# Kernel optimization log

Measured on AMD Instinct MI355X. Metric: run time of the kernel, lower is better.

## Reference

```python
import jax, jax.numpy as jnp
import numpy as np

DELTA_V = 0.5
DELTA_D = 1.5
ALPHA = 1.0
BETA = 1.0
GAMMA = 0.001
K = 64  # max number of instance ids per batch element


def _safe_sqrt(sq):
    # sqrt with zero-safe gradient: exact where sq > 0, returns 0 otherwise
    pos = sq > 0
    return jnp.sqrt(jnp.where(pos, sq, 1.0)) * pos.astype(sq.dtype)


def setup_inputs() -> dict:
    key = jax.random.key(0)
    k1, k2 = jax.random.split(key)
    B, N, D = 16, 65536, 32
    embeddings = jax.random.normal(k1, (B, N, D), dtype=jnp.float32)
    instance_ids = jax.random.randint(k2, (B, N), 0, K, dtype=jnp.int32)
    mask = jnp.ones((B, N), dtype=bool)
    return {"embeddings": embeddings, "instance_ids": instance_ids, "mask": mask}


def reference(embeddings, instance_ids, mask):
    B, N, D = embeddings.shape
    f32 = embeddings.dtype
    valid = mask & (instance_ids >= 0)
    # flat segment id per point; invalid points go to dump segment B*K
    batch_off = jnp.arange(B, dtype=jnp.int32)[:, None] * K
    seg = jnp.where(valid, batch_off + instance_ids, B * K).reshape(-1)
    w = valid.reshape(-1).astype(f32)
    flat = embeddings.reshape(-1, D)

    # per-instance sums / counts -> means  (segment reduce, memory-bound)
    sums = jax.ops.segment_sum(flat * w[:, None], seg, num_segments=B * K + 1)[: B * K]
    counts = jax.ops.segment_sum(w, seg, num_segments=B * K + 1)[: B * K]
    means_flat = sums / jnp.maximum(counts, 1.0)[:, None]  # (B*K, D)
    present = (counts > 0).reshape(B, K)                   # (B, K)
    num_inst = present.sum(-1).astype(f32)                 # (B,)
    valid_b = (num_inst >= 2).astype(f32)                  # batches counted as samples

    # ---- variance (pull) loss ----
    seg_clip = jnp.minimum(seg, B * K - 1)
    diff = flat - means_flat[seg_clip]                     # (B*N, D)
    dist = _safe_sqrt((diff * diff).sum(-1))
    pen = jnp.maximum(dist - DELTA_V, 0.0) ** 2 * w
    inst_pen = jax.ops.segment_sum(pen, seg, num_segments=B * K + 1)[: B * K]
    inst_pen = (inst_pen / jnp.maximum(counts, 1.0)).reshape(B, K)
    var_b = (inst_pen * present).sum(-1) / jnp.maximum(num_inst, 1.0)

    # ---- distance (push) loss: pairwise over instance means ----
    means = means_flat.reshape(B, K, D)
    dsq = ((means[:, :, None, :] - means[:, None, :, :]) ** 2).sum(-1)  # (B, K, K)
    iu = jnp.arange(K)
    pair_m = present[:, :, None] & present[:, None, :] & (iu[:, None] < iu[None, :])
    pair_mf = pair_m.astype(f32)
    pdist = _safe_sqrt(jnp.where(pair_m, dsq, 1.0)) * pair_mf
    pen2 = jnp.maximum(2.0 * DELTA_D - pdist, 0.0) ** 2 * pair_mf
    num_pairs = num_inst * (num_inst - 1.0) / 2.0
    dist_b = pen2.sum((1, 2)) / jnp.maximum(num_pairs, 1.0)

    # ---- regularization loss ----
    mnorm = _safe_sqrt((means * means).sum(-1)) * present.astype(f32)  # (B, K)
    reg_b = mnorm.sum(-1) / jnp.maximum(num_inst, 1.0)

    denom = jnp.maximum(valid_b.sum(), 1.0)
    var_loss = (var_b * valid_b).sum() / denom
    dist_loss = (dist_b * valid_b).sum() / denom
    reg_loss = (reg_b * valid_b).sum() / denom
    total = ALPHA * var_loss + BETA * dist_loss + GAMMA * reg_loss
    return jnp.stack([total, var_loss, dist_loss, reg_loss])
```

## Files before the change

kernel.cpp:

```cpp
#include <hip/hip_runtime.h>
#include <cstdint>

#define BB 16
#define NN 65536
#define DD 32
#define KK 64
#define DELTA_V 0.5f
#define DELTA_D 1.5f

typedef short bf16x8 __attribute__((ext_vector_type(8)));
typedef float f32x16 __attribute__((ext_vector_type(16)));

__device__ __forceinline__ short f2bf(float x) {
    union { float f; unsigned u; } v; v.f = x;
    const unsigned r = v.u + 0x7FFFu + ((v.u >> 16) & 1u);
    return (short)(r >> 16);
}

#define K1_BPB 64
#define K1_PPB 1024

__global__ __launch_bounds__(256, 4) void k_accum(
    const float* __restrict__ emb, const int* __restrict__ ids,
    const int* __restrict__ mask, float* __restrict__ parts,
    float* __restrict__ pcnt)
{
    __shared__ float tb[4][64][36];
    __shared__ float lc2[4][KK];
    const int tid  = threadIdx.x;
    const int w    = tid >> 6, lane = tid & 63;
    const int half = lane >> 5, d32 = lane & 31;
    const int pl   = lane >> 3;
    const int pc   = lane & 7;
    const int b    = blockIdx.x >> 6;
    const int blk  = blockIdx.x & 63;
    const size_t pw = (size_t)b * NN + (size_t)blk * K1_PPB + (size_t)w * 256;

    f32x16 acc0 = {}, acc1 = {};
    int c0 = 0, c1 = 0;
    const int m0 = d32, m1 = d32 + 32;
    float (*T)[36] = tb[w];

    for (int s = 0; s < 4; ++s) {
        const size_t ps = pw + s * 64;
        const float4* ep4 = (const float4*)(emb + ps * DD);
        float4 r[8];
#pragma unroll
        for (int i = 0; i < 8; ++i) r[i] = ep4[i * 64 + lane];
        const int idr = ids[ps + lane];
        const int mkr = mask[ps + lane];
        const int vid = (mkr != 0 && (unsigned)idr < KK) ? idr : -1;

#pragma unroll
        for (int i = 0; i < 8; ++i)
            *(float4*)&T[i * 8 + pl][4 * pc] = r[i];

#pragma unroll
        for (int q = 0; q < 4; ++q) {
            bf16x8 bfB, a0, a1;
#pragma unroll
            for (int e = 0; e < 8; ++e) {
                bfB[e] = f2bf(T[q * 16 + 8 * half + e][d32]);
                const int s_lo = __builtin_amdgcn_readlane(vid, q * 16 + e);
                const int s_hi = __builtin_amdgcn_readlane(vid, q * 16 + 8 + e);
                const int sel  = half ? s_hi : s_lo;
                const bool h0 = (sel == m0), h1 = (sel == m1);
                a0[e] = h0 ? (short)0x3F80 : (short)0;
                a1[e] = h1 ? (short)0x3F80 : (short)0;
                c0 += h0 ? 1 : 0;
                c1 += h1 ? 1 : 0;
            }
            acc0 = __builtin_amdgcn_mfma_f32_32x32x16_bf16(a0, bfB, acc0, 0, 0, 0);
            acc1 = __builtin_amdgcn_mfma_f32_32x32x16_bf16(a1, bfB, acc1, 0, 0, 0);
        }
    }

#pragma unroll
    for (int r = 0; r < 16; ++r) {
        const int mrow = (r & 3) + 8 * (r >> 2) + 4 * half;
        T[mrow][d32]      = acc0[r];
        T[32 + mrow][d32] = acc1[r];
    }
    c0 += __shfl_down(c0, 32);
    c1 += __shfl_down(c1, 32);
    if (lane < 32) { lc2[w][lane] = (float)c0; lc2[w][lane + 32] = (float)c1; }
    __syncthreads();

    float* pb = parts + (size_t)blockIdx.x * (KK * DD);
    for (int i = tid; i < KK * DD; i += 256) {
        const int row = i >> 5, col = i & 31;
        pb[i] = tb[0][row][col] + tb[1][row][col] + tb[2][row][col] + tb[3][row][col];
    }
    if (tid < KK)
        pcnt[(size_t)blockIdx.x * KK + tid] =
            lc2[0][tid] + lc2[1][tid] + lc2[2][tid] + lc2[3][tid];
}

__global__ __launch_bounds__(256) void k_reduce_push(
    const float* __restrict__ parts, const float* __restrict__ pcnt,
    float* __restrict__ mu, float* __restrict__ regb,
    float* __restrict__ distb)
{
    const int b = blockIdx.x;
    const int tid = threadIdx.x;
    __shared__ float lm[KK][DD + 1];
    __shared__ float lcnt[KK];
    __shared__ float red[4];

    if (tid < KK) {
        float s = 0.f;
        for (int j = 0; j < K1_BPB; ++j)
            s += pcnt[((size_t)b * K1_BPB + j) * KK + tid];
        lcnt[tid] = s;
        mu[(size_t)b * KK * 36 + tid * 36 + 32] = s;
        mu[(size_t)b * KK * 36 + tid * 36 + 33] = 1.f / fmaxf(s, 1.f);
    }
    __syncthreads();

    for (int e = tid; e < KK * DD; e += 256) {
        float s = 0.f;
        for (int j = 0; j < K1_BPB; ++j)
            s += parts[((size_t)b * K1_BPB + j) * (KK * DD) + e];
        const int k = e >> 5, d = e & 31;
        const float m = s / fmaxf(lcnt[k], 1.f);
        lm[k][d] = m;
        mu[(size_t)b * KK * 36 + k * 36 + d] = m;
    }
    __syncthreads();

    float ninst = 0.f;
    if (tid < KK) {
        const float c = lcnt[tid];
        const float pres = (c > 0.f) ? 1.f : 0.f;
        float sq = 0.f;
#pragma unroll
        for (int d = 0; d < DD; ++d) { const float m = lm[tid][d]; sq = fmaf(m, m, sq); }
        float nm = ((sq > 0.f) ? sqrtf(sq) : 0.f) * pres;
        float pn = pres;
        for (int off = 32; off; off >>= 1) {
            pn += __shfl_down(pn, off);
            nm += __shfl_down(nm, off);
        }
        if (tid == 0) {
            ninst = pn;
            regb[b] = nm / fmaxf(pn, 1.f);
        }
    }

    float acc = 0.f;
    for (int idx = tid; idx < KK * KK; idx += 256) {
        const int i = idx >> 6, j = idx & 63;
        if (i < j && lcnt[i] > 0.f && lcnt[j] > 0.f) {
            float dsq = 0.f;
#pragma unroll
            for (int d = 0; d < DD; ++d) {
                const float df = lm[i][d] - lm[j][d];
                dsq = fmaf(df, df, dsq);
            }
            const float pd = (dsq > 0.f) ? sqrtf(dsq) : 0.f;
            const float pen = fmaxf(2.f * DELTA_D - pd, 0.f);
            acc = fmaf(pen, pen, acc);
        }
    }
    for (int off = 32; off; off >>= 1) acc += __shfl_down(acc, off);
    if ((tid & 63) == 0) red[tid >> 6] = acc;
    __syncthreads();
    if (tid == 0) {
        const float tot = red[0] + red[1] + red[2] + red[3];
        const float np = ninst * (ninst - 1.f) * 0.5f;
        distb[b] = tot / fmaxf(np, 1.f);
    }
}

#define K2_BPB 64
#define K2_PTS 1024

__global__ __launch_bounds__(256) void k_pull(
    const float* __restrict__ emb, const int* __restrict__ ids,
    const int* __restrict__ mask, const float* __restrict__ mu,
    float* __restrict__ varpart)
{
    __shared__ float smu[KK][36];
    __shared__ float red[4];
    const int tid = threadIdx.x;
    const int w = tid >> 6, lane = tid & 63;
    const int pl = lane >> 3;
    const int pc = lane & 7;
    const int b   = blockIdx.x >> 6;
    const int blk = blockIdx.x & 63;

    const float* mub = mu + (size_t)b * KK * 36;
    for (int i = tid; i < KK * 36; i += 256) ((float*)smu)[i] = mub[i];
    __syncthreads();

    const size_t p0 = (size_t)b * NN + (size_t)blk * K2_PTS + (size_t)w * 256;
    float accv = 0.f;
    for (int t = 0; t < 4; ++t) {
        const size_t pt0 = p0 + t * 64;
        const int idr = ids[pt0 + lane];
        const int mkr = mask[pt0 + lane];
        const int vid = (mkr != 0 && (unsigned)idr < KK) ? idr : -1;
        const float4* ep4 = (const float4*)(emb + pt0 * DD);
#pragma unroll
        for (int g = 0; g < 8; ++g) {
            const float4 x = ep4[g * 64 + lane];
            const int sid = __shfl(vid, g * 8 + pl);
            const int row = (sid >= 0) ? sid : 0;
            const float4 m4 = *(const float4*)&smu[row][4 * pc];
            float dsq;
            {
                float a = x.x - m4.x; dsq = a * a;
                a = x.y - m4.y; dsq = fmaf(a, a, dsq);
                a = x.z - m4.z; dsq = fmaf(a, a, dsq);
                a = x.w - m4.w; dsq = fmaf(a, a, dsq);
            }
            dsq += __shfl_xor(dsq, 1);
            dsq += __shfl_xor(dsq, 2);
            dsq += __shfl_xor(dsq, 4);
            if (pc == 0 && sid >= 0) {
                const float dist = (dsq > 0.f) ? sqrtf(dsq) : 0.f;
                float pen = fmaxf(dist - DELTA_V, 0.f);
                accv = fmaf(pen * pen, smu[row][33], accv);
            }
        }
    }
    for (int off = 32; off; off >>= 1) accv += __shfl_down(accv, off);
    if (lane == 0) red[w] = accv;
    __syncthreads();
    if (tid == 0)
        varpart[blockIdx.x] = red[0] + red[1] + red[2] + red[3];
}

__global__ __launch_bounds__(64) void k_final(
    const float* __restrict__ mu, const float* __restrict__ varpart,
    const float* __restrict__ regb, const float* __restrict__ distb,
    float* __restrict__ out)
{
    const int tid = threadIdx.x;
    __shared__ float s_var[BB], s_valid[BB];
    if (tid < BB) {
        const int b = tid;
        float ni = 0.f;
        for (int k = 0; k < KK; ++k)
            ni += (mu[(size_t)b * KK * 36 + k * 36 + 32] > 0.f) ? 1.f : 0.f;
        float vs = 0.f;
        for (int j = 0; j < K2_BPB; ++j) vs += varpart[b * K2_BPB + j];
        s_var[tid]   = vs / fmaxf(ni, 1.f);
        s_valid[tid] = (ni >= 2.f) ? 1.f : 0.f;
    }
    __syncthreads();
    if (tid == 0) {
        float denom = 0.f, v = 0.f, d = 0.f, r = 0.f;
        for (int b = 0; b < BB; ++b) {
            const float vb = s_valid[b];
            denom += vb;
            v += s_var[b] * vb;
            d += distb[b] * vb;
            r += regb[b] * vb;
        }
        denom = fmaxf(denom, 1.f);
        v /= denom; d /= denom; r /= denom;
        out[0] = v + d + 0.001f * r;
        out[1] = v;
        out[2] = d;
        out[3] = r;
    }
}

extern "C" void kernel_launch(void* const* d_in, const int* in_sizes, int n_in,
                              void* d_out, int out_size, void* d_ws, size_t ws_size,
                              hipStream_t stream)
{
    const float* emb  = (const float*)d_in[0];
    const int*   ids  = (const int*)d_in[1];
    const int*   mask = (const int*)d_in[2];

    float* ws      = (float*)d_ws;
    float* parts   = ws;
    float* pcnt    = parts + (size_t)BB * K1_BPB * KK * DD;
    float* mu      = pcnt + (size_t)BB * K1_BPB * KK;
    float* varpart = mu + (size_t)BB * KK * 36;
    float* regb    = varpart + BB * K2_BPB;
    float* distb   = regb + BB;

    k_accum<<<BB * K1_BPB, 256, 0, stream>>>(emb, ids, mask, parts, pcnt);
    k_reduce_push<<<BB, 256, 0, stream>>>(parts, pcnt, mu, regb, distb);
    k_pull<<<BB * K2_BPB, 256, 0, stream>>>(emb, ids, mask, mu, varpart);
    k_final<<<1, 64, 0, stream>>>(mu, varpart, regb, distb, (float*)d_out);
}
```

Measured before the change: 96.03 us.

## Load embeddings directly into registers with double-buffered prefetch in accumulate kernel

The accumulate kernel no longer stages embeddings through LDS and transposes them there. Each lane now loads the 32 scalars it needs for the MFMA B operand straight from global memory. The next 64-point slice is prefetched into a second register buffer while the current one is processed, to overlap load latency with MFMA work. The cost is scalar (non-vectorized) strided global loads and 64 extra live registers, which may reduce occupancy. The variance kernel change is cosmetic.

```diff
diff --git a/kernel.cpp b/kernel.cpp
--- a/kernel.cpp
+++ b/kernel.cpp
@@ -25,13 +25,11 @@
     const int* __restrict__ mask, float* __restrict__ parts,
     float* __restrict__ pcnt)
 {
-    __shared__ float tb[4][64][36];
-    __shared__ float lc2[4][KK];
+    __shared__ float tbl[4][64][32];
+    __shared__ float lc2[4][64];
     const int tid  = threadIdx.x;
     const int w    = tid >> 6, lane = tid & 63;
     const int half = lane >> 5, d32 = lane & 31;
-    const int pl   = lane >> 3;
-    const int pc   = lane & 7;
     const int b    = blockIdx.x >> 6;
     const int blk  = blockIdx.x & 63;
     const size_t pw = (size_t)b * NN + (size_t)blk * K1_PPB + (size_t)w * 256;
@@ -39,28 +37,36 @@
     f32x16 acc0 = {}, acc1 = {};
     int c0 = 0, c1 = 0;
     const int m0 = d32, m1 = d32 + 32;
-    float (*T)[36] = tb[w];
-
+
+    const int* idsb = ids + pw;
+    const int* mskb = mask + pw;
+    const float* eb = emb + (pw + (size_t)half * 8) * DD + d32;
+
+    float xa[32], xb[32];
+    int idr, mkr;
+#pragma unroll
+    for (int j = 0; j < 32; ++j)
+        xa[j] = eb[(size_t)(((j >> 3) * 16) + (j & 7)) * DD];
+    idr = idsb[lane]; mkr = mskb[lane];
+
+#pragma unroll
     for (int s = 0; s < 4; ++s) {
-        const size_t ps = pw + s * 64;
-        const float4* ep4 = (const float4*)(emb + ps * DD);
-        float4 r[8];
-#pragma unroll
-        for (int i = 0; i < 8; ++i) r[i] = ep4[i * 64 + lane];
-        const int idr = ids[ps + lane];
-        const int mkr = mask[ps + lane];
+        int idr2 = 0, mkr2 = 0;
+        if (s < 3) {
+            const float* eb2 = eb + (size_t)(s + 1) * 64 * DD;
+#pragma unroll
+            for (int j = 0; j < 32; ++j)
+                xb[j] = eb2[(size_t)(((j >> 3) * 16) + (j & 7)) * DD];
+            idr2 = idsb[(s + 1) * 64 + lane];
+            mkr2 = mskb[(s + 1) * 64 + lane];
+        }
         const int vid = (mkr != 0 && (unsigned)idr < KK) ? idr : -1;
-
-#pragma unroll
-        for (int i = 0; i < 8; ++i)
-            *(float4*)&T[i * 8 + pl][4 * pc] = r[i];
-
 #pragma unroll
         for (int q = 0; q < 4; ++q) {
             bf16x8 bfB, a0, a1;
 #pragma unroll
             for (int e = 0; e < 8; ++e) {
-                bfB[e] = f2bf(T[q * 16 + 8 * half + e][d32]);
+                bfB[e] = f2bf(xa[q * 8 + e]);
                 const int s_lo = __builtin_amdgcn_readlane(vid, q * 16 + e);
                 const int s_hi = __builtin_amdgcn_readlane(vid, q * 16 + 8 + e);
                 const int sel  = half ? s_hi : s_lo;
@@ -73,23 +79,29 @@
             acc0 = __builtin_amdgcn_mfma_f32_32x32x16_bf16(a0, bfB, acc0, 0, 0, 0);
             acc1 = __builtin_amdgcn_mfma_f32_32x32x16_bf16(a1, bfB, acc1, 0, 0, 0);
         }
+        if (s < 3) {
+#pragma unroll
+            for (int j = 0; j < 32; ++j) xa[j] = xb[j];
+            idr = idr2; mkr = mkr2;
+        }
     }
 
 #pragma unroll
     for (int r = 0; r < 16; ++r) {
         const int mrow = (r & 3) + 8 * (r >> 2) + 4 * half;
-        T[mrow][d32]      = acc0[r];
-        T[32 + mrow][d32] = acc1[r];
+        tbl[w][mrow][d32]      = acc0[r];
+        tbl[w][32 + mrow][d32] = acc1[r];
     }
     c0 += __shfl_down(c0, 32);
     c1 += __shfl_down(c1, 32);
     if (lane < 32) { lc2[w][lane] = (float)c0; lc2[w][lane + 32] = (float)c1; }
     __syncthreads();
 
-    float* pb = parts + (size_t)blockIdx.x * (KK * DD);
-    for (int i = tid; i < KK * DD; i += 256) {
+    float* pb = parts + (size_t)blockIdx.x * 2048;
+    for (int i = tid; i < 2048; i += 256) {
         const int row = i >> 5, col = i & 31;
-        pb[i] = tb[0][row][col] + tb[1][row][col] + tb[2][row][col] + tb[3][row][col];
+        pb[i] = tbl[0][row][col] + tbl[1][row][col]
+              + tbl[2][row][col] + tbl[3][row][col];
     }
     if (tid < KK)
         pcnt[(size_t)blockIdx.x * KK + tid] =
@@ -207,13 +219,10 @@
             const int sid = __shfl(vid, g * 8 + pl);
             const int row = (sid >= 0) ? sid : 0;
             const float4 m4 = *(const float4*)&smu[row][4 * pc];
-            float dsq;
-            {
-                float a = x.x - m4.x; dsq = a * a;
-                a = x.y - m4.y; dsq = fmaf(a, a, dsq);
-                a = x.z - m4.z; dsq = fmaf(a, a, dsq);
-                a = x.w - m4.w; dsq = fmaf(a, a, dsq);
-            }
+            float a = x.x - m4.x; float dsq = a * a;
+            a = x.y - m4.y; dsq = fmaf(a, a, dsq);
+            a = x.z - m4.z; dsq = fmaf(a, a, dsq);
+            a = x.w - m4.w; dsq = fmaf(a, a, dsq);
             dsq += __shfl_xor(dsq, 1);
             dsq += __shfl_xor(dsq, 2);
             dsq += __shfl_xor(dsq, 4);
```

Result: faster. 92.41 us (-3.8%).
